# Optimization experiments

Measured on AMD Instinct MI355X. Metric: run time of the kernel, lower is better.

## Reference

```python
import jax, jax.numpy as jnp
import numpy as np

DIM = 1024
NUM_HEADS = 16
HEAD_DIM = DIM // NUM_HEADS  # 64
MAX_LABELS = 8
B, SQ, SKV = 2, 2048, 2048


def setup_inputs() -> dict:
    key = jax.random.key(0)
    ks = jax.random.split(key, 12)
    s = 0.02
    return {
        "visual_features": jax.random.normal(ks[0], (B, SQ, DIM), jnp.float32),
        "audio_features": jax.random.normal(ks[1], (B, SKV, DIM), jnp.float32),
        "audio_labels": jax.random.randint(ks[2], (B,), 0, MAX_LABELS),
        "Wq": jax.random.normal(ks[3], (DIM, DIM), jnp.float32) * s,
        "bq": jnp.zeros((DIM,), jnp.float32),
        "Wk": jax.random.normal(ks[4], (DIM, DIM), jnp.float32) * s,
        "bk": jnp.zeros((DIM,), jnp.float32),
        "Wv": jax.random.normal(ks[5], (DIM, DIM), jnp.float32) * s,
        "bv": jnp.zeros((DIM,), jnp.float32),
        "Wo": jax.random.normal(ks[6], (DIM, DIM), jnp.float32) * s,
        "bo": jnp.zeros((DIM,), jnp.float32),
        "label_emb": jax.random.normal(ks[7], (MAX_LABELS, HEAD_DIM), jnp.float32),
    }


def _lrope_emb(label_emb, labels, seq_len, dtype):
    # inv_freq over head_dim (buffer, recomputed)
    inv_freq = 1.0 / (10000.0 ** (jnp.arange(0, HEAD_DIM, 2, dtype=jnp.float32) / HEAD_DIM))
    pos = jnp.arange(seq_len, dtype=dtype)
    freqs = jnp.outer(pos, inv_freq)                       # [S, hd/2]
    emb = jnp.concatenate([jnp.sin(freqs), jnp.cos(freqs)], axis=-1)  # [S, hd]
    lab = label_emb[labels]                                # [B, hd]
    return emb[None, :, :] * lab[:, None, :]               # [B, S, hd]


def reference(visual_features, audio_features, audio_labels,
              Wq, bq, Wk, bk, Wv, bv, Wo, bo, label_emb):
    b, sq, _ = visual_features.shape
    skv = audio_features.shape[1]
    scale = HEAD_DIM ** -0.5

    q = visual_features @ Wq.T + bq                        # [B, Sq, D]
    k = audio_features @ Wk.T + bk                         # [B, Skv, D]
    v = audio_features @ Wv.T + bv

    q = q.reshape(b, sq, NUM_HEADS, HEAD_DIM)
    k = k.reshape(b, skv, NUM_HEADS, HEAD_DIM)
    v = v.reshape(b, skv, NUM_HEADS, HEAD_DIM)

    # L-RoPE additive embedding on K (per-head broadcast of the head_dim-sized emb)
    emb = _lrope_emb(label_emb, audio_labels, skv, k.dtype)  # [B, Skv, hd]
    k = k + emb[:, :, None, :]

    scores = jnp.einsum('bqhd,bkhd->bhqk', q, k) * scale   # [B, H, Sq, Skv]
    attn = jax.nn.softmax(scores, axis=-1)                 # dropout = identity (eval)
    out = jnp.einsum('bhqk,bkhd->bqhd', attn, v)           # [B, Sq, H, hd]
    out = out.reshape(b, sq, DIM)
    return out @ Wo.T + bo
```

## Files before the change

### kernel.cpp

```cpp
#include <hip/hip_runtime.h>
#include <hip/hip_bf16.h>


typedef short s16x8 __attribute__((ext_vector_type(8)));
typedef float f32x4 __attribute__((ext_vector_type(4)));

__device__ __forceinline__ short f2bf(float f) {
    unsigned u = __float_as_uint(f);
    u = u + 0x7fffu + ((u >> 16) & 1u);
    return (short)(u >> 16);
}

__device__ __forceinline__ unsigned cvtpk(float lo, float hi) {
    unsigned r;
    asm volatile("v_cvt_pk_bf16_f32 %0, %1, %2" : "=v"(r) : "v"(lo), "v"(hi));
    return r;
}

#define GLDS16(g, l)                                                          \
    __builtin_amdgcn_global_load_lds(                                         \
        (const __attribute__((address_space(1))) void*)(g),                   \
        (__attribute__((address_space(3))) void*)(l), 16, 0, 0)

__global__ __launch_bounds__(256)
void cvt_all(const float* __restrict__ vis, const float* __restrict__ aud,
             const float* __restrict__ Wq, const float* __restrict__ Wk,
             const float* __restrict__ Wv, const float* __restrict__ Wo,
             short* __restrict__ visB, short* __restrict__ audB,
             short* __restrict__ WqB, short* __restrict__ WkB,
             short* __restrict__ WvB, short* __restrict__ WoB)
{
    const int bid = blockIdx.x;
    const float* src; short* dst; int vec0;
    if (bid < 2048)      { src = vis; dst = visB; vec0 = bid * 256; }
    else if (bid < 4096) { src = aud; dst = audB; vec0 = (bid - 2048) * 256; }
    else {
        const int r = bid - 4096, w = r >> 9, lb = r & 511;
        vec0 = lb * 256;
        if      (w == 0) { src = Wq; dst = WqB; }
        else if (w == 1) { src = Wk; dst = WkB; }
        else if (w == 2) { src = Wv; dst = WvB; }
        else             { src = Wo; dst = WoB; }
    }
    const int i = (vec0 + threadIdx.x) * 8;
    float4 a = *(const float4*)(src + i);
    float4 b = *(const float4*)(src + i + 4);
    s16x8 o;
    o[0]=f2bf(a.x); o[1]=f2bf(a.y); o[2]=f2bf(a.z); o[3]=f2bf(a.w);
    o[4]=f2bf(b.x); o[5]=f2bf(b.y); o[6]=f2bf(b.z); o[7]=f2bf(b.w);
    *(s16x8*)(dst + i) = o;
}

__global__ __launch_bounds__(256)
void gemm_qkv(const short* __restrict__ visB, const short* __restrict__ audB,
              const short* __restrict__ WqB, const short* __restrict__ WkB,
              const short* __restrict__ WvB,
              const float* __restrict__ bq, const float* __restrict__ bk,
              const float* __restrict__ bv,
              short* __restrict__ outQ, short* __restrict__ outK,
              short* __restrict__ outVt,
              const int* __restrict__ labels, const float* __restrict__ lemb)
{
    __shared__ __align__(16) short As[2][64 * 64];
    __shared__ __align__(16) short Bs[2][128 * 64];
    const int tid  = threadIdx.x;
    const int lane = tid & 63;
    const int wid  = tid >> 6;
    const int q15  = lane & 15;
    const int hi   = lane >> 4;
    const int z    = blockIdx.z;
    const int rowBase = blockIdx.y * 64;
    const int colBase = blockIdx.x * 128;
    const int wr = (wid >> 1) * 32;
    const int wc = (wid & 1) * 64;
    const short* X = (z == 0) ? visB : audB;
    const short* W = (z == 0) ? WqB : (z == 1) ? WkB : WvB;
    const float* bias = (z == 0) ? bq : (z == 1) ? bk : bv;

    f32x4 acc[2][4] = {};

    auto stage = [&](int buf, int k0) {
        #pragma unroll
        for (int c = 0; c < 2; ++c) {
            const int u   = c * 256 + tid;
            const int row = u >> 3;
            const int k8a = (u & 7) ^ (row & 7);
            GLDS16(X + (size_t)(rowBase + row) * 1024 + k0 + k8a * 8,
                   &As[buf][(c * 256 + wid * 64) * 8]);
        }
        #pragma unroll
        for (int c = 0; c < 4; ++c) {
            const int u   = c * 256 + tid;
            const int row = u >> 3;
            const int k8a = (u & 7) ^ (row & 7);
            GLDS16(W + (size_t)(colBase + row) * 1024 + k0 + k8a * 8,
                   &Bs[buf][(c * 256 + wid * 64) * 8]);
        }
    };

    stage(0, 0);
    __syncthreads();

    for (int t = 0; t < 16; ++t) {
        const int cur = t & 1;
        if (t < 15) stage(cur ^ 1, (t + 1) * 64);
        #pragma unroll
        for (int ks = 0; ks < 2; ++ks) {
            const int kb = ks * 64 + (hi << 4);
            s16x8 af[2], bfv[4];
            #pragma unroll
            for (int m = 0; m < 2; ++m) {
                const int row = wr + m * 16 + q15;
                af[m] = *(const s16x8*)((const char*)&As[cur][0] + row * 128 + (kb ^ ((row & 7) << 4)));
            }
            #pragma unroll
            for (int n = 0; n < 4; ++n) {
                const int row = wc + n * 16 + q15;
                bfv[n] = *(const s16x8*)((const char*)&Bs[cur][0] + row * 128 + (kb ^ ((row & 7) << 4)));
            }
            #pragma unroll
            for (int m = 0; m < 2; ++m)
                #pragma unroll
                for (int n = 0; n < 4; ++n)
                    acc[m][n] = __builtin_amdgcn_mfma_f32_16x16x32_bf16(af[m], bfv[n], acc[m][n], 0, 0, 0);
        }
        __syncthreads();
    }

    if (z == 2) {
        __syncthreads();
        char* tb = (char*)&As[0][0] + wid * 4096;
        const int b  = rowBase >> 11;
        const int h  = (colBase + wc) >> 6;
        const int kvbase = (rowBase & 2047) + wr;
        #pragma unroll
        for (int m = 0; m < 2; ++m) {
            #pragma unroll
            for (int r = 0; r < 4; ++r) {
                const int kvl = m * 16 + hi * 4 + r;
                #pragma unroll
                for (int n = 0; n < 4; ++n) {
                    const int hd = n * 16 + q15;
                    const float v = acc[m][n][r] + bias[colBase + wc + hd];
                    *(short*)(tb + hd * 64 + ((kvl * 2) ^ ((hd & 3) << 4))) = f2bf(v);
                }
            }
        }
        asm volatile("s_waitcnt lgkmcnt(0)" ::: "memory");
        #pragma unroll
        for (int c = 0; c < 4; ++c) {
            const int u  = c * 64 + lane;
            const int hd = u >> 2;
            const int kc = u & 3;
            s16x8 vv = *(const s16x8*)(tb + hd * 64 + ((kc * 16) ^ ((hd & 3) << 4)));
            *(s16x8*)(outVt + ((size_t)(b * 16 + h) * 64 + hd) * 2048 + kvbase + kc * 8) = vv;
        }
    } else {
        short* Co = (z == 0) ? outQ : outK;
        #pragma unroll
        for (int m = 0; m < 2; ++m) {
            #pragma unroll
            for (int r = 0; r < 4; ++r) {
                const int grow = rowBase + wr + m * 16 + hi * 4 + r;
                #pragma unroll
                for (int n = 0; n < 4; ++n) {
                    const int gcol = colBase + wc + n * 16 + q15;
                    float v = acc[m][n][r] + bias[gcol];
                    if (z == 0) {
                        v *= 0.125f;
                    } else {
                        const int bb = grow >> 11;
                        const int ss = grow & 2047;
                        const int hd = gcol & 63;
                        const int fi = hd & 31;
                        const float ang = (float)ss * __expf((float)fi * (-9.210340371976184f / 32.0f));
                        const float tr  = (hd < 32) ? sinf(ang) : cosf(ang);
                        v += tr * lemb[labels[bb] * 64 + hd];
                    }
                    Co[(size_t)grow * 1024 + gcol] = f2bf(v);
                }
            }
        }
    }
}

__global__ __launch_bounds__(256)
void gemm_out(const short* __restrict__ X, const short* __restrict__ W,
              const float* __restrict__ bias, float* __restrict__ Cf)
{
    __shared__ __align__(16) short As[2][64 * 64];
    __shared__ __align__(16) short Bs[2][128 * 64];
    const int tid  = threadIdx.x;
    const int lane = tid & 63;
    const int wid  = tid >> 6;
    const int q15  = lane & 15;
    const int hi   = lane >> 4;
    const int rowBase = blockIdx.y * 64;
    const int colBase = blockIdx.x * 128;
    const int wr = (wid >> 1) * 32;
    const int wc = (wid & 1) * 64;

    f32x4 acc[2][4] = {};

    auto stage = [&](int buf, int k0) {
        #pragma unroll
        for (int c = 0; c < 2; ++c) {
            const int u   = c * 256 + tid;
            const int row = u >> 3;
            const int k8a = (u & 7) ^ (row & 7);
            GLDS16(X + (size_t)(rowBase + row) * 1024 + k0 + k8a * 8,
                   &As[buf][(c * 256 + wid * 64) * 8]);
        }
        #pragma unroll
        for (int c = 0; c < 4; ++c) {
            const int u   = c * 256 + tid;
            const int row = u >> 3;
            const int k8a = (u & 7) ^ (row & 7);
            GLDS16(W + (size_t)(colBase + row) * 1024 + k0 + k8a * 8,
                   &Bs[buf][(c * 256 + wid * 64) * 8]);
        }
    };

    stage(0, 0);
    __syncthreads();

    for (int t = 0; t < 16; ++t) {
        const int cur = t & 1;
        if (t < 15) stage(cur ^ 1, (t + 1) * 64);
        #pragma unroll
        for (int ks = 0; ks < 2; ++ks) {
            const int kb = ks * 64 + (hi << 4);
            s16x8 af[2], bfv[4];
            #pragma unroll
            for (int m = 0; m < 2; ++m) {
                const int row = wr + m * 16 + q15;
                af[m] = *(const s16x8*)((const char*)&As[cur][0] + row * 128 + (kb ^ ((row & 7) << 4)));
            }
            #pragma unroll
            for (int n = 0; n < 4; ++n) {
                const int row = wc + n * 16 + q15;
                bfv[n] = *(const s16x8*)((const char*)&Bs[cur][0] + row * 128 + (kb ^ ((row & 7) << 4)));
            }
            #pragma unroll
            for (int m = 0; m < 2; ++m)
                #pragma unroll
                for (int n = 0; n < 4; ++n)
                    acc[m][n] = __builtin_amdgcn_mfma_f32_16x16x32_bf16(af[m], bfv[n], acc[m][n], 0, 0, 0);
        }
        __syncthreads();
    }

    #pragma unroll
    for (int m = 0; m < 2; ++m) {
        #pragma unroll
        for (int r = 0; r < 4; ++r) {
            const int grow = rowBase + wr + m * 16 + hi * 4 + r;
            #pragma unroll
            for (int n = 0; n < 4; ++n) {
                const int gcol = colBase + wc + n * 16 + q15;
                Cf[(size_t)grow * 1024 + gcol] = acc[m][n][r] + bias[gcol];
            }
        }
    }
}

__global__ __launch_bounds__(256)
void attn_fwd(const short* __restrict__ Q, const short* __restrict__ K,
              const short* __restrict__ Vt, short* __restrict__ AO)
{
    __shared__ __align__(16) short Ks[2][64 * 64];
    __shared__ __align__(16) short Vs[2][64 * 64];
    __shared__ __align__(16) short Ps[4][16 * 64];
    const int tid  = threadIdx.x;
    const int lane = tid & 63;
    const int wid  = tid >> 6;
    const int q15  = lane & 15;
    const int hi   = lane >> 4;
    const int qt = blockIdx.x;
    const int bh = blockIdx.y;
    const int b  = bh >> 4, h = bh & 15;
    const int qrow0 = b * 2048 + qt * 64;
    const int hoff  = h * 64;
    const short* Kb = K + (size_t)b * 2048 * 1024 + hoff;
    const short* Vb = Vt + (size_t)bh * 64 * 2048;
    char* pw = (char*)&Ps[wid][0];
    const int psw = (q15 & 7) << 4;

    s16x8 qf[2];
    {
        const int qr = qrow0 + wid * 16 + q15;
        const short* qp = Q + (size_t)qr * 1024 + hoff + hi * 8;
        qf[0] = *(const s16x8*)(qp);
        qf[1] = *(const s16x8*)(qp + 32);
    }

    auto stage = [&](int buf, int kv0) {
        #pragma unroll
        for (int c = 0; c < 2; ++c) {
            const int ub  = c * 256 + wid * 64;
            const int u   = ub + lane;
            const int row = u >> 3;
            const int k8  = (u & 7) ^ (row & 7);
            GLDS16(Kb + (size_t)(kv0 + row) * 1024 + k8 * 8, &Ks[buf][ub * 8]);
            GLDS16(Vb + (size_t)row * 2048 + kv0 + k8 * 8,   &Vs[buf][ub * 8]);
        }
    };

    float mrun = -1e30f, lsum = 0.f;
    f32x4 o[4] = {};

    stage(0, 0);
    __syncthreads();

    for (int t = 0; t < 32; ++t) {
        const int cur = t & 1;
        if (t < 31) stage(cur ^ 1, (t + 1) * 64);

        f32x4 s[4] = {};
        #pragma unroll
        for (int ks = 0; ks < 2; ++ks) {
            const int kb = ks * 64 + (hi << 4);
            #pragma unroll
            for (int n = 0; n < 4; ++n) {
                const int row = n * 16 + q15;
                s16x8 kf = *(const s16x8*)((const char*)&Ks[cur][0] + row * 128 + (kb ^ ((row & 7) << 4)));
                s[n] = __builtin_amdgcn_mfma_f32_16x16x32_bf16(kf, qf[ks], s[n], 0, 0, 0);
            }
        }

        float pm = s[0][0];
        #pragma unroll
        for (int n = 0; n < 4; ++n)
            #pragma unroll
            for (int r = 0; r < 4; ++r) pm = fmaxf(pm, s[n][r]);
        if (__any(pm > mrun + 8.0f)) {
            float t2 = fmaxf(pm, __shfl_xor(pm, 16));
            t2 = fmaxf(t2, __shfl_xor(t2, 32));
            const float mn = fmaxf(mrun, t2);
            const float al = __expf(mrun - mn);
            mrun = mn;
            lsum *= al;
            float alq[4];
            #pragma unroll
            for (int r = 0; r < 4; ++r) alq[r] = __shfl(al, hi * 4 + r);
            #pragma unroll
            for (int n = 0; n < 4; ++n)
                #pragma unroll
                for (int r = 0; r < 4; ++r) o[n][r] *= alq[r];
        }
        #pragma unroll
        for (int n = 0; n < 4; ++n) {
            float p0 = __expf(s[n][0] - mrun);
            float p1 = __expf(s[n][1] - mrun);
            float p2 = __expf(s[n][2] - mrun);
            float p3 = __expf(s[n][3] - mrun);
            lsum += (p0 + p1) + (p2 + p3);
            uint2 pk;
            pk.x = cvtpk(p0, p1);
            pk.y = cvtpk(p2, p3);
            *(uint2*)(pw + q15 * 128 + ((n * 32 + hi * 8) ^ psw)) = pk;
        }
        asm volatile("s_waitcnt lgkmcnt(0)" ::: "memory");

        #pragma unroll
        for (int ks = 0; ks < 2; ++ks) {
            const int kb = ks * 64 + (hi << 4);
            s16x8 pa = *(const s16x8*)(pw + q15 * 128 + ((ks * 64 + hi * 16) ^ psw));
            #pragma unroll
            for (int n = 0; n < 4; ++n) {
                const int row = n * 16 + q15;
                s16x8 vb = *(const s16x8*)((const char*)&Vs[cur][0] + row * 128 + (kb ^ ((row & 7) << 4)));
                o[n] = __builtin_amdgcn_mfma_f32_16x16x32_bf16(pa, vb, o[n], 0, 0, 0);
            }
        }
        __syncthreads();
    }

    float tt = lsum;
    tt += __shfl_xor(tt, 16);
    tt += __shfl_xor(tt, 32);
    const float inv = 1.0f / tt;
    float invq[4];
    #pragma unroll
    for (int r = 0; r < 4; ++r) invq[r] = __shfl(inv, hi * 4 + r);
    #pragma unroll
    for (int r = 0; r < 4; ++r) {
        const int grow = qrow0 + wid * 16 + hi * 4 + r;
        #pragma unroll
        for (int n = 0; n < 4; ++n) {
            const int gcol = hoff + n * 16 + q15;
            AO[(size_t)grow * 1024 + gcol] = f2bf(o[n][r] * invq[r]);
        }
    }
}

extern "C" void kernel_launch(void* const* d_in, const int* in_sizes, int n_in,
                              void* d_out, int out_size, void* d_ws, size_t ws_size,
                              hipStream_t stream) {
    const float* vis    = (const float*)d_in[0];
    const float* aud    = (const float*)d_in[1];
    const int*   labels = (const int*)d_in[2];
    const float* Wq = (const float*)d_in[3];  const float* bq = (const float*)d_in[4];
    const float* Wk = (const float*)d_in[5];  const float* bk = (const float*)d_in[6];
    const float* Wv = (const float*)d_in[7];  const float* bv = (const float*)d_in[8];
    const float* Wo = (const float*)d_in[9];  const float* bo = (const float*)d_in[10];
    const float* lemb = (const float*)d_in[11];

    short* wsQ   = (short*)d_ws;
    short* wsK   = wsQ  + 4194304;
    short* wsVt  = wsK  + 4194304;
    short* wsAO  = wsVt + 4194304;
    short* visB  = wsAO + 4194304;
    short* audB  = visB + 4194304;
    short* WqB   = audB + 4194304;
    short* WkB   = WqB  + 1048576;
    short* WvB   = WkB  + 1048576;
    short* WoB   = WvB  + 1048576;
    float* out   = (float*)d_out;

    cvt_all<<<6144, 256, 0, stream>>>(vis, aud, Wq, Wk, Wv, Wo,
                                      visB, audB, WqB, WkB, WvB, WoB);
    gemm_qkv<<<dim3(8, 64, 3), 256, 0, stream>>>(visB, audB, WqB, WkB, WvB,
                                                 bq, bk, bv, wsQ, wsK, wsVt,
                                                 labels, lemb);
    attn_fwd<<<dim3(32, 32), 256, 0, stream>>>(wsQ, wsK, wsVt, wsAO);
    gemm_out<<<dim3(8, 64), 256, 0, stream>>>(wsAO, WoB, bo, out);
}
```

Before: 248.9 us.

## Process 32 query rows per wave in attention to reuse K/V tiles

Each wave in the attention kernel now handles two 16-row query fragments instead of one, so a block covers 128 query rows and the grid halves. Every K and V fragment read from LDS feeds two MFMAs, and each staged K/V tile serves twice as many queries, which cuts global and LDS traffic per unit of work. The cost is more registers for the doubled accumulators and softmax state, and only 512 blocks, which may lower occupancy and latency hiding on a large GPU.

After: 244.4 us. No clear change (-1.8%).

```diff
diff --git a/kernel.cpp b/kernel.cpp
--- a/kernel.cpp
+++ b/kernel.cpp
@@ -270,7 +270,7 @@
 {
     __shared__ __align__(16) short Ks[2][64 * 64];
     __shared__ __align__(16) short Vs[2][64 * 64];
-    __shared__ __align__(16) short Ps[4][16 * 64];
+    __shared__ __align__(16) short Ps[4][32 * 64];
     const int tid  = threadIdx.x;
     const int lane = tid & 63;
     const int wid  = tid >> 6;
@@ -279,19 +279,20 @@
     const int qt = blockIdx.x;
     const int bh = blockIdx.y;
     const int b  = bh >> 4, h = bh & 15;
-    const int qrow0 = b * 2048 + qt * 64;
+    const int qrow0 = b * 2048 + qt * 128 + wid * 32;
     const int hoff  = h * 64;
     const short* Kb = K + (size_t)b * 2048 * 1024 + hoff;
     const short* Vb = Vt + (size_t)bh * 64 * 2048;
     char* pw = (char*)&Ps[wid][0];
     const int psw = (q15 & 7) << 4;
 
-    s16x8 qf[2];
-    {
-        const int qr = qrow0 + wid * 16 + q15;
+    s16x8 qf[2][2];
+    #pragma unroll
+    for (int f = 0; f < 2; ++f) {
+        const int qr = qrow0 + f * 16 + q15;
         const short* qp = Q + (size_t)qr * 1024 + hoff + hi * 8;
-        qf[0] = *(const s16x8*)(qp);
-        qf[1] = *(const s16x8*)(qp + 32);
+        qf[f][0] = *(const s16x8*)(qp);
+        qf[f][1] = *(const s16x8*)(qp + 32);
     }
 
     auto stage = [&](int buf, int kv0) {
@@ -306,8 +307,8 @@
         }
     };
 
-    float mrun = -1e30f, lsum = 0.f;
-    f32x4 o[4] = {};
+    float mrun[2] = {-1e30f, -1e30f}, lsum[2] = {0.f, 0.f};
+    f32x4 o[2][4] = {};
 
     stage(0, 0);
     __syncthreads();
@@ -316,7 +317,7 @@
         const int cur = t & 1;
         if (t < 31) stage(cur ^ 1, (t + 1) * 64);
 
-        f32x4 s[4] = {};
+        f32x4 s[2][4] = {};
         #pragma unroll
         for (int ks = 0; ks < 2; ++ks) {
             const int kb = ks * 64 + (hi << 4);
@@ -324,72 +325,88 @@
             for (int n = 0; n < 4; ++n) {
                 const int row = n * 16 + q15;
                 s16x8 kf = *(const s16x8*)((const char*)&Ks[cur][0] + row * 128 + (kb ^ ((row & 7) << 4)));
-                s[n] = __builtin_amdgcn_mfma_f32_16x16x32_bf16(kf, qf[ks], s[n], 0, 0, 0);
-            }
-        }
-
-        float pm = s[0][0];
-        #pragma unroll
-        for (int n = 0; n < 4; ++n)
-            #pragma unroll
-            for (int r = 0; r < 4; ++r) pm = fmaxf(pm, s[n][r]);
-        if (__any(pm > mrun + 8.0f)) {
-            float t2 = fmaxf(pm, __shfl_xor(pm, 16));
-            t2 = fmaxf(t2, __shfl_xor(t2, 32));
-            const float mn = fmaxf(mrun, t2);
-            const float al = __expf(mrun - mn);
-            mrun = mn;
-            lsum *= al;
-            float alq[4];
-            #pragma unroll
-            for (int r = 0; r < 4; ++r) alq[r] = __shfl(al, hi * 4 + r);
+                s[0][n] = __builtin_amdgcn_mfma_f32_16x16x32_bf16(kf, qf[0][ks], s[0][n], 0, 0, 0);
+                s[1][n] = __builtin_amdgcn_mfma_f32_16x16x32_bf16(kf, qf[1][ks], s[1][n], 0, 0, 0);
+            }
+        }
+
+        float pm[2];
+        #pragma unroll
+        for (int f = 0; f < 2; ++f) {
+            pm[f] = s[f][0][0];
             #pragma unroll
             for (int n = 0; n < 4; ++n)
                 #pragma unroll
-                for (int r = 0; r < 4; ++r) o[n][r] *= alq[r];
-        }
-        #pragma unroll
-        for (int n = 0; n < 4; ++n) {
-            float p0 = __expf(s[n][0] - mrun);
-            float p1 = __expf(s[n][1] - mrun);
-            float p2 = __expf(s[n][2] - mrun);
-            float p3 = __expf(s[n][3] - mrun);
-            lsum += (p0 + p1) + (p2 + p3);
-            uint2 pk;
-            pk.x = cvtpk(p0, p1);
-            pk.y = cvtpk(p2, p3);
-            *(uint2*)(pw + q15 * 128 + ((n * 32 + hi * 8) ^ psw)) = pk;
+                for (int r = 0; r < 4; ++r) pm[f] = fmaxf(pm[f], s[f][n][r]);
+        }
+        if (__any((pm[0] > mrun[0] + 8.0f) || (pm[1] > mrun[1] + 8.0f))) {
+            #pragma unroll
+            for (int f = 0; f < 2; ++f) {
+                float t2 = fmaxf(pm[f], __shfl_xor(pm[f], 16));
+                t2 = fmaxf(t2, __shfl_xor(t2, 32));
+                const float mn = fmaxf(mrun[f], t2);
+                const float al = __expf(mrun[f] - mn);
+                mrun[f] = mn;
+                lsum[f] *= al;
+                float alq[4];
+                #pragma unroll
+                for (int r = 0; r < 4; ++r) alq[r] = __shfl(al, hi * 4 + r);
+                #pragma unroll
+                for (int n = 0; n < 4; ++n)
+                    #pragma unroll
+                    for (int r = 0; r < 4; ++r) o[f][n][r] *= alq[r];
+            }
+        }
+        #pragma unroll
+        for (int f = 0; f < 2; ++f) {
+            #pragma unroll
+            for (int n = 0; n < 4; ++n) {
+                float p0 = __expf(s[f][n][0] - mrun[f]);
+                float p1 = __expf(s[f][n][1] - mrun[f]);
+                float p2 = __expf(s[f][n][2] - mrun[f]);
+                float p3 = __expf(s[f][n][3] - mrun[f]);
+                lsum[f] += (p0 + p1) + (p2 + p3);
+                uint2 pk;
+                pk.x = cvtpk(p0, p1);
+                pk.y = cvtpk(p2, p3);
+                *(uint2*)(pw + (f * 16 + q15) * 128 + ((n * 32 + hi * 8) ^ psw)) = pk;
+            }
         }
         asm volatile("s_waitcnt lgkmcnt(0)" ::: "memory");
 
         #pragma unroll
         for (int ks = 0; ks < 2; ++ks) {
             const int kb = ks * 64 + (hi << 4);
-            s16x8 pa = *(const s16x8*)(pw + q15 * 128 + ((ks * 64 + hi * 16) ^ psw));
+            s16x8 pa0 = *(const s16x8*)(pw + (q15) * 128 + ((ks * 64 + hi * 16) ^ psw));
+            s16x8 pa1 = *(const s16x8*)(pw + (16 + q15) * 128 + ((ks * 64 + hi * 16) ^ psw));
             #pragma unroll
             for (int n = 0; n < 4; ++n) {
                 const int row = n * 16 + q15;
                 s16x8 vb = *(const s16x8*)((const char*)&Vs[cur][0] + row * 128 + (kb ^ ((row & 7) << 4)));
-                o[n] = __builtin_amdgcn_mfma_f32_16x16x32_bf16(pa, vb, o[n], 0, 0, 0);
+                o[0][n] = __builtin_amdgcn_mfma_f32_16x16x32_bf16(pa0, vb, o[0][n], 0, 0, 0);
+                o[1][n] = __builtin_amdgcn_mfma_f32_16x16x32_bf16(pa1, vb, o[1][n], 0, 0, 0);
             }
         }
         __syncthreads();
     }
 
-    float tt = lsum;
-    tt += __shfl_xor(tt, 16);
-    tt += __shfl_xor(tt, 32);
-    const float inv = 1.0f / tt;
-    float invq[4];
     #pragma unroll
-    for (int r = 0; r < 4; ++r) invq[r] = __shfl(inv, hi * 4 + r);
-    #pragma unroll
-    for (int r = 0; r < 4; ++r) {
-        const int grow = qrow0 + wid * 16 + hi * 4 + r;
-        #pragma unroll
-        for (int n = 0; n < 4; ++n) {
-            const int gcol = hoff + n * 16 + q15;
-            AO[(size_t)grow * 1024 + gcol] = f2bf(o[n][r] * invq[r]);
+    for (int f = 0; f < 2; ++f) {
+        float tt = lsum[f];
+        tt += __shfl_xor(tt, 16);
+        tt += __shfl_xor(tt, 32);
+        const float inv = 1.0f / tt;
+        float invq[4];
+        #pragma unroll
+        for (int r = 0; r < 4; ++r) invq[r] = __shfl(inv, hi * 4 + r);
+        #pragma unroll
+        for (int r = 0; r < 4; ++r) {
+            const int grow = qrow0 + f * 16 + hi * 4 + r;
+            #pragma unroll
+            for (int n = 0; n < 4; ++n) {
+                const int gcol = hoff + n * 16 + q15;
+                AO[(size_t)grow * 1024 + gcol] = f2bf(o[f][n][r] * invq[r]);
+            }
         }
     }
 }
@@ -423,6 +440,6 @@
     gemm_qkv<<<dim3(8, 64, 3), 256, 0, stream>>>(visB, audB, WqB, WkB, WvB,
                                                  bq, bk, bv, wsQ, wsK, wsVt,
                                                  labels, lemb);
-    attn_fwd<<<dim3(32, 32), 256, 0, stream>>>(wsQ, wsK, wsVt, wsAO);
+    attn_fwd<<<dim3(16, 32), 256, 0, stream>>>(wsQ, wsK, wsVt, wsAO);
     gemm_out<<<dim3(8, 64), 256, 0, stream>>>(wsAO, WoB, bo, out);
 }
```
